# Kernel optimization log

Hardware: AMD Instinct MI355X
Metric: run time of the kernel (lower is better)

The kernel has to match this reference:

```python
import jax, jax.numpy as jnp
import numpy as np

B, S, H, NH = 2, 2048, 2048, 16
HD = H // NH  # 128


def setup_inputs() -> dict:
    key = jax.random.key(0)
    ks = jax.random.split(key, 6)
    x = jax.random.normal(ks[0], (B, S, H), dtype=jnp.float32)
    # causal additive mask: 0 on/below diagonal, -1e9 above
    causal = jnp.triu(jnp.full((S, S), -1e9, dtype=jnp.float32), k=1)
    attention_mask = causal[None, None, :, :]  # [1,1,S,S]
    # ALiBi: per-head slope * key position, broadcast over queries
    slopes = 2.0 ** (-8.0 * (jnp.arange(NH, dtype=jnp.float32) + 1) / NH)
    alibi = (-slopes[:, None] * jnp.arange(S, dtype=jnp.float32)[None, :])
    alibi = alibi[None, :, None, :]  # [1,NH,1,S]
    scale = 0.02
    Wq = jax.random.normal(ks[1], (H, H), dtype=jnp.float32) * scale
    Wk = jax.random.normal(ks[2], (H, H), dtype=jnp.float32) * scale
    Wv = jax.random.normal(ks[3], (H, H), dtype=jnp.float32) * scale
    Wo = jax.random.normal(ks[4], (H, H), dtype=jnp.float32) * scale
    return {"x": x, "attention_mask": attention_mask, "alibi": alibi,
            "Wq": Wq, "Wk": Wk, "Wv": Wv, "Wo": Wo}


def reference(x, attention_mask, alibi, Wq, Wk, Wv, Wo):
    b, s, _ = x.shape
    # nn.Linear(y) = y @ W.T
    q = (x @ Wq.T).reshape(b, s, NH, HD).transpose(0, 2, 1, 3)  # [b,h,s,d]
    k = (x @ Wk.T).reshape(b, s, NH, HD).transpose(0, 2, 1, 3)
    v = (x @ Wv.T).reshape(b, s, NH, HD).transpose(0, 2, 1, 3)
    scores = jnp.einsum('bhqd,bhkd->bhqk', q, k) / jnp.sqrt(jnp.float32(HD))
    scores = scores + alibi + attention_mask
    attn = jax.nn.softmax(scores, axis=-1)
    out = jnp.einsum('bhqk,bhkd->bhqd', attn, v)
    out = out.transpose(0, 2, 1, 3).reshape(b, s, H)
    return out @ Wo.T
```

## Files before the change

### kernel.cpp

```cpp
#include <hip/hip_runtime.h>

typedef unsigned short u16;
typedef float f32x4 __attribute__((ext_vector_type(4)));
typedef short s16x8 __attribute__((ext_vector_type(8)));
typedef short s16x4 __attribute__((ext_vector_type(4)));
typedef unsigned short u16x4 __attribute__((ext_vector_type(4)));

#define S_LEN 2048
#define HDIM 2048
#define NHEADS 16
#define HEAD_DIM 128

__device__ __forceinline__ u16 f2bf(float f) {
    unsigned u = __builtin_bit_cast(unsigned, f);
    u += 0x7FFFu + ((u >> 16) & 1u);
    return (u16)(u >> 16);
}

__device__ __forceinline__ void gload_lds16(const u16* g, u16* l) {
    __builtin_amdgcn_global_load_lds(
        (const __attribute__((address_space(1))) unsigned int*)(const void*)g,
        (__attribute__((address_space(3))) unsigned int*)(void*)l, 16, 0, 0);
}

#define PBAR __builtin_amdgcn_s_barrier()
#define SGB0 __builtin_amdgcn_sched_barrier(0)

__device__ __forceinline__ void tr_read16(const u16* bptr, s16x4* o) {
    auto p = (const __attribute__((address_space(3))) u16*)(const void*)bptr;
    asm volatile(
        "ds_read_b64_tr_b16 %0, %16\n\t"
        "ds_read_b64_tr_b16 %1, %16 offset:1024\n\t"
        "ds_read_b64_tr_b16 %2, %16 offset:128\n\t"
        "ds_read_b64_tr_b16 %3, %16 offset:1152\n\t"
        "ds_read_b64_tr_b16 %4, %16 offset:256\n\t"
        "ds_read_b64_tr_b16 %5, %16 offset:1280\n\t"
        "ds_read_b64_tr_b16 %6, %16 offset:384\n\t"
        "ds_read_b64_tr_b16 %7, %16 offset:1408\n\t"
        "ds_read_b64_tr_b16 %8, %16 offset:512\n\t"
        "ds_read_b64_tr_b16 %9, %16 offset:1536\n\t"
        "ds_read_b64_tr_b16 %10, %16 offset:640\n\t"
        "ds_read_b64_tr_b16 %11, %16 offset:1664\n\t"
        "ds_read_b64_tr_b16 %12, %16 offset:768\n\t"
        "ds_read_b64_tr_b16 %13, %16 offset:1792\n\t"
        "ds_read_b64_tr_b16 %14, %16 offset:896\n\t"
        "ds_read_b64_tr_b16 %15, %16 offset:1920\n\t"
        "s_waitcnt lgkmcnt(0)"
        : "=&v"(o[0]), "=&v"(o[1]), "=&v"(o[2]), "=&v"(o[3]),
          "=&v"(o[4]), "=&v"(o[5]), "=&v"(o[6]), "=&v"(o[7]),
          "=&v"(o[8]), "=&v"(o[9]), "=&v"(o[10]), "=&v"(o[11]),
          "=&v"(o[12]), "=&v"(o[13]), "=&v"(o[14]), "=&v"(o[15])
        : "v"(p));
    __builtin_amdgcn_sched_barrier(0);
}

__global__ void cvt_bf16(const float* __restrict__ in, u16* __restrict__ out, int n4, float scale) {
    int i = blockIdx.x * blockDim.x + threadIdx.x;
    int stride = gridDim.x * blockDim.x;
    for (; i < n4; i += stride) {
        float4 f = ((const float4*)in)[i];
        u16x4 r;
        r.x = f2bf(f.x * scale); r.y = f2bf(f.y * scale);
        r.z = f2bf(f.z * scale); r.w = f2bf(f.w * scale);
        *(u16x4*)(out + (size_t)i * 4) = r;
    }
}

__global__ void cvt_w4(const float* __restrict__ w0, const float* __restrict__ w1,
                       const float* __restrict__ w2, const float* __restrict__ w3,
                       u16* __restrict__ out, float scale0) {
    const int n4each = (HDIM * HDIM) / 4;
    int b = blockIdx.x;
    int which = b >> 11;
    const float* src = which == 0 ? w0 : which == 1 ? w1 : which == 2 ? w2 : w3;
    float sc = which == 0 ? scale0 : 1.0f;
    u16* dst = out + (size_t)which * (HDIM * HDIM);
    int i = (b & 2047) * 256 + threadIdx.x;
    const int stride = 2048 * 256;
    for (; i < n4each; i += stride) {
        float4 f = ((const float4*)src)[i];
        u16x4 r;
        r.x = f2bf(f.x * sc); r.y = f2bf(f.y * sc);
        r.z = f2bf(f.z * sc); r.w = f2bf(f.w * sc);
        *(u16x4*)(dst + (size_t)i * 4) = r;
    }
}

template<int OUT_F32>
__global__ __launch_bounds__(512, 2) void gemm_ring(const u16* __restrict__ A, const u16* __restrict__ Bw,
                                                    void* __restrict__ C0, void* __restrict__ C1,
                                                    void* __restrict__ C2, int M, int N, int K) {
    __shared__ u16 lds[3 * 24576];

    const int bid = blockIdx.x;
    const int xcd = bid & 7;
    const int q = bid >> 3;
    const int rr = q & 31, sc0 = q >> 5;
    const int bm = xcd * 4 + (rr & 3);
    const int bn = sc0 * 8 + (rr >> 2);

    const int t = threadIdx.x, lane = t & 63, w = t >> 6;
    const int wm = w >> 2, wn = w & 3;
    const int rqg = lane >> 4, rl = lane & 15;

    const size_t rowA0 = (size_t)bm * 128;
    const int colB0 = bn << 8;

    const u16* srcA[2]; int dA[2];
#pragma unroll
    for (int i = 0; i < 2; ++i) {
        int c = t + i * 512;
        int row = c >> 3, ch = c & 7;
        srcA[i] = A + (rowA0 + row) * (size_t)K + ((ch ^ (row & 7)) << 3);
        dA[i] = c * 8;
    }
    const u16* srcB[4]; int dB[4];
#pragma unroll
    for (int i = 0; i < 4; ++i) {
        int c = t + i * 512;
        int row = c >> 3, ch = c & 7;
        srcB[i] = Bw + (size_t)(colB0 + row) * (size_t)K + ((ch ^ (row & 7)) << 3);
        dB[i] = c * 8;
    }

    auto stage = [&](int tile, int s) {
        const size_t go = (size_t)tile * 64;
        u16* base = &lds[s * 24576];
#pragma unroll
        for (int i = 0; i < 2; ++i) gload_lds16(srcA[i] + go, base + dA[i]);
#pragma unroll
        for (int i = 0; i < 4; ++i) gload_lds16(srcB[i] + go, base + 8192 + dB[i]);
    };

    const int chv[2] = { ((0 + rqg) ^ (rl & 7)) << 3, ((4 + rqg) ^ (rl & 7)) << 3 };
    const int arow = wm * 64, brow = wn * 64;

    f32x4 acc[4][4] = {};

    const int NT = K >> 6;

    stage(0, 0); stage(1, 1);
    asm volatile("s_waitcnt vmcnt(6)" ::: "memory");
    PBAR;

    int s = 0;
    for (int tt = 0; tt < NT; ++tt) {
        const u16* sA = &lds[s * 24576];
        const u16* sB = sA + 8192;

        s16x8 af[4][2], bf[4][2];
#pragma unroll
        for (int m = 0; m < 4; ++m)
#pragma unroll
            for (int k = 0; k < 2; ++k)
                af[m][k] = *(const s16x8*)&sA[(arow + m * 16 + rl) * 64 + chv[k]];
#pragma unroll
        for (int n = 0; n < 4; ++n)
#pragma unroll
            for (int k = 0; k < 2; ++k)
                bf[n][k] = *(const s16x8*)&sB[(brow + n * 16 + rl) * 64 + chv[k]];

        int s2 = s + 2; if (s2 >= 3) s2 -= 3;
        if (tt + 2 < NT) stage(tt + 2, s2);
        SGB0;

        __builtin_amdgcn_s_setprio(1);
#pragma unroll
        for (int m = 0; m < 4; ++m)
#pragma unroll
            for (int n = 0; n < 4; ++n)
#pragma unroll
                for (int k = 0; k < 2; ++k)
                    acc[m][n] = __builtin_amdgcn_mfma_f32_16x16x32_bf16(af[m][k], bf[n][k], acc[m][n], 0, 0, 0);
        __builtin_amdgcn_s_setprio(0);

        if (tt + 2 < NT)      { asm volatile("s_waitcnt vmcnt(6)" ::: "memory"); }
        else if (tt + 1 < NT) { asm volatile("s_waitcnt vmcnt(0)" ::: "memory"); }
        PBAR;
        ++s; if (s == 3) s = 0;
    }

    const int mat = colB0 >> 11;
    void* Csel = mat == 0 ? C0 : mat == 1 ? C1 : C2;
    const int colb = (colB0 & 2047) + wn * 64;
#pragma unroll
    for (int m = 0; m < 4; ++m) {
#pragma unroll
        for (int n = 0; n < 4; ++n) {
#pragma unroll
            for (int j = 0; j < 4; ++j) {
                size_t row = rowA0 + wm * 64 + m * 16 + rqg * 4 + j;
                size_t col = colb + n * 16 + rl;
                float v = acc[m][n][j];
                if (OUT_F32) ((float*)Csel)[row * 2048 + col] = v;
                else ((u16*)Csel)[row * 2048 + col] = f2bf(v);
            }
        }
    }
}

__global__ __launch_bounds__(512) void attn_kernel(const u16* __restrict__ Q, const u16* __restrict__ Kb,
                                                   const u16* __restrict__ Vb,
                                                   const float* __restrict__ alibi,
                                                   u16* __restrict__ O) {
    __shared__ u16 ldsKV[3 * 16384];
    __shared__ u16 lP[8][16 * 80];

    const int bid = blockIdx.x;
    const int bh = bid & 31;
    const int p = bid >> 5;
    const int h = bh & 15, b = bh >> 4;
    const int t = threadIdx.x, lane = t & 63, w = t >> 6;
    const int rqg = lane >> 4, rl = lane & 15;

    const size_t bS = (size_t)b * S_LEN;
    const size_t hOff = (size_t)h * HEAD_DIM;

    const u16* ksrc[2]; const u16* vsrc[2]; int cdst[2];
#pragma unroll
    for (int i = 0; i < 2; ++i) {
        int c = t + i * 512;
        int krow = c >> 4, kch = c & 15;
        ksrc[i] = Kb + (bS + krow) * HDIM + hOff + ((kch ^ (krow & 7)) << 3);
        int vkey = ((c >> 6) << 2) + ((c >> 1) & 3);
        int vd = (((c >> 3) & 7) << 4) + ((c & 1) << 3);
        vsrc[i] = Vb + (bS + vkey) * HDIM + hOff + vd;
        cdst[i] = c * 8;
    }

    auto stageKV = [&](int tile, int s) {
        const size_t goff = (size_t)tile * 64 * HDIM;
        u16* base = &ldsKV[s * 16384];
#pragma unroll
        for (int i = 0; i < 2; ++i) {
            gload_lds16(ksrc[i] + goff, base + cdst[i]);
            gload_lds16(vsrc[i] + goff, base + 8192 + cdst[i]);
        }
    };

    const float mslope2 = alibi[(size_t)h * S_LEN + 1] * 1.4426950408889634f;

    s16x8 ones;
#pragma unroll
    for (int i = 0; i < 8; ++i) ones[i] = (short)0x3F80;

    for (int sidx = 0; sidx < 2; ++sidx) {
        const int qt = sidx ? (15 - p) : p;
        const int q0w = qt * 128 + w * 16;

        const size_t baseQ = (bS + q0w + rl) * HDIM + hOff;
        s16x8 qf[4];
#pragma unroll
        for (int kk = 0; kk < 4; ++kk)
            qf[kk] = *(const s16x8*)(Q + baseQ + kk * 32 + rqg * 8);

        float m[4];
        f32x4 o[8]; f32x4 osum = {0.f, 0.f, 0.f, 0.f};
#pragma unroll
        for (int j = 0; j < 4; ++j) m[j] = -1e30f;
#pragma unroll
        for (int n = 0; n < 8; ++n) o[n] = (f32x4){0.f, 0.f, 0.f, 0.f};

        const int nkt = 2 * qt + 2;
        const int my_last = 2 * qt + (w >> 2);
        u16* lPw = lP[w];

        stageKV(0, 0); stageKV(1, 1);
        asm volatile("s_waitcnt vmcnt(4)" ::: "memory");
        PBAR;

        int s = 0;
        for (int kt = 0; kt < nkt; ++kt) {
            int s2 = s + 2; if (s2 >= 3) s2 -= 3;
            if (kt + 2 < nkt) stageKV(kt + 2, s2);

            if (kt <= my_last) {
                const int k0 = kt * 64;
                const u16* kbase = &ldsKV[s * 16384];

                f32x4 sfr[4] = {};
#pragma unroll
                for (int kk = 0; kk < 4; ++kk) {
#pragma unroll
                    for (int nt = 0; nt < 4; ++nt) {
                        int row = nt * 16 + rl;
                        int off = row * 256 + ((kk * 64 + rqg * 16) ^ ((row & 7) << 4));
                        s16x8 kf = *(const s16x8*)((const char*)kbase + off);
                        sfr[nt] = __builtin_amdgcn_mfma_f32_16x16x32_bf16(qf[kk], kf, sfr[nt], 0, 0, 0);
                    }
                }

                const bool diag = (kt == my_last);
                float scv[4][4];
                float thr0 = m[0] + 8.f, thr1 = m[1] + 8.f, thr2 = m[2] + 8.f, thr3 = m[3] + 8.f;
                int small = 1;
#pragma unroll
                for (int nt = 0; nt < 4; ++nt) {
                    int key = k0 + nt * 16 + rl;
                    float al = mslope2 * (float)key;
#pragma unroll
                    for (int j = 0; j < 4; ++j) {
                        float v = sfr[nt][j] + al;
                        if (diag) {
                            int qrow = q0w + rqg * 4 + j;
                            v = (key <= qrow) ? v : -1e30f;
                        }
                        scv[nt][j] = v;
                        float thr = (j == 0) ? thr0 : (j == 1) ? thr1 : (j == 2) ? thr2 : thr3;
                        small &= (v <= thr) ? 1 : 0;
                    }
                }
                if (!__all(small)) {
                    float rmax[4];
#pragma unroll
                    for (int j = 0; j < 4; ++j)
                        rmax[j] = fmaxf(fmaxf(scv[0][j], scv[1][j]), fmaxf(scv[2][j], scv[3][j]));
#pragma unroll
                    for (int off = 1; off < 16; off <<= 1) {
#pragma unroll
                        for (int j = 0; j < 4; ++j) rmax[j] = fmaxf(rmax[j], __shfl_xor(rmax[j], off));
                    }
#pragma unroll
                    for (int j = 0; j < 4; ++j) {
                        float mn = fmaxf(m[j], rmax[j]);
                        float fac = exp2f(m[j] - mn);
                        m[j] = mn;
                        osum[j] *= fac;
#pragma unroll
                        for (int n = 0; n < 8; ++n) o[n][j] *= fac;
                    }
                }

#pragma unroll
                for (int nt = 0; nt < 4; ++nt) {
#pragma unroll
                    for (int j = 0; j < 4; ++j) {
                        float pv = exp2f(scv[nt][j] - m[j]);
                        lPw[(rqg * 4 + j) * 80 + nt * 16 + rl] = f2bf(pv);
                    }
                }

                const u16* lVbase = &ldsKV[s * 16384] + 8192 + rqg * 1024 + rl * 4;
#pragma unroll
                for (int kk = 0; kk < 2; ++kk) {
                    s16x8 pf = *(const s16x8*)&lPw[rl * 80 + kk * 32 + rqg * 8];
                    osum = __builtin_amdgcn_mfma_f32_16x16x32_bf16(pf, ones, osum, 0, 0, 0);
                    s16x4 tr[16];
                    tr_read16(lVbase + kk * 4096, tr);
#pragma unroll
                    for (int n = 0; n < 8; ++n) {
                        s16x8 vf = __builtin_shufflevector(tr[2 * n], tr[2 * n + 1], 0, 1, 2, 3, 4, 5, 6, 7);
                        o[n] = __builtin_amdgcn_mfma_f32_16x16x32_bf16(pf, vf, o[n], 0, 0, 0);
                    }
                }
            }

            if (kt + 2 < nkt)      { asm volatile("s_waitcnt vmcnt(4)" ::: "memory"); }
            else if (kt + 1 < nkt) { asm volatile("s_waitcnt vmcnt(0)" ::: "memory"); }
            PBAR;
            ++s; if (s == 3) s = 0;
        }

        float inv[4];
#pragma unroll
        for (int j = 0; j < 4; ++j) inv[j] = 1.0f / osum[j];
#pragma unroll
        for (int n = 0; n < 8; ++n) {
#pragma unroll
            for (int j = 0; j < 4; ++j) {
                size_t row = bS + q0w + rqg * 4 + j;
                O[row * HDIM + hOff + n * 16 + rl] = f2bf(o[n][j] * inv[j]);
            }
        }
    }
}

extern "C" void kernel_launch(void* const* d_in, const int* in_sizes, int n_in,
                              void* d_out, int out_size, void* d_ws, size_t ws_size,
                              hipStream_t stream) {
    (void)in_sizes; (void)n_in; (void)out_size; (void)ws_size;
    const float* x     = (const float*)d_in[0];
    const float* alibi = (const float*)d_in[2];
    const float* Wq    = (const float*)d_in[3];
    const float* Wk    = (const float*)d_in[4];
    const float* Wv    = (const float*)d_in[5];
    const float* Wo    = (const float*)d_in[6];
    float* out = (float*)d_out;

    char* ws = (char*)d_ws;
    u16* xb  = (u16*)(ws + 0);
    u16* wqb = (u16*)(ws + 16777216);
    u16* Qb  = (u16*)(ws + 50331648);
    u16* Kv  = Qb + 8388608;
    u16* Vv  = Kv + 8388608;
    u16* Ob  = Vv + 8388608;
    u16* wob = wqb + 3 * 4194304;

    const int M = 2 * S_LEN;
    const int K = HDIM;

    const float qscale = 0.08838834764831845f * 1.4426950408889634f;
    cvt_bf16<<<4096, 256, 0, stream>>>(x, xb, (2 * S_LEN * HDIM) / 4, 1.0f);
    cvt_w4<<<8192, 256, 0, stream>>>(Wq, Wk, Wv, Wo, wqb, qscale);

    gemm_ring<0><<<(M / 128) * (3 * HDIM / 256), 512, 0, stream>>>(xb, wqb, Qb, Kv, Vv, M, 3 * HDIM, K);

    attn_kernel<<<2 * NHEADS * 8, 512, 0, stream>>>(Qb, Kv, Vv, alibi, Ob);

    gemm_ring<1><<<(M / 128) * (HDIM / 256), 512, 0, stream>>>(Ob, wob, out, out, out, M, HDIM, K);
}
```

Measured before the change: 254.2 us.

## Switch GEMM to 256x128 tiles with intra-block split-K across warp halves

Changes the GEMM block tile from 128x256 to 256x128 and splits the 64-wide K slice between two groups of four waves, each computing a 128x64 sub-tile over half the K chunk. The partial sums from the second group are reduced through LDS before the epilogue. The prefetch for the next stage is also issued before the fragment loads, with an explicit lgkmcnt wait. This halves the number of fragment loads per MFMA relative to accumulator size and raises accumulator registers per wave, at the cost of an LDS reduction and a barrier at the end, plus a changed block-to-XCD mapping.

```diff
diff --git a/kernel.cpp b/kernel.cpp
--- a/kernel.cpp
+++ b/kernel.cpp
@@ -95,47 +95,47 @@
     const int bid = blockIdx.x;
     const int xcd = bid & 7;
     const int q = bid >> 3;
-    const int rr = q & 31, sc0 = q >> 5;
-    const int bm = xcd * 4 + (rr & 3);
-    const int bn = sc0 * 8 + (rr >> 2);
+    const int bm = xcd * 2 + (q & 1);
+    const int bn = q >> 1;
 
     const int t = threadIdx.x, lane = t & 63, w = t >> 6;
-    const int wm = w >> 2, wn = w & 3;
+    const int kk = w >> 2;
+    const int wm = (w >> 1) & 1, wn = w & 1;
     const int rqg = lane >> 4, rl = lane & 15;
 
-    const size_t rowA0 = (size_t)bm * 128;
-    const int colB0 = bn << 8;
-
-    const u16* srcA[2]; int dA[2];
-#pragma unroll
-    for (int i = 0; i < 2; ++i) {
+    const size_t rowA0 = (size_t)bm * 256;
+    const int colB0 = bn << 7;
+
+    const u16* srcA[4]; int dA[4];
+#pragma unroll
+    for (int i = 0; i < 4; ++i) {
         int c = t + i * 512;
         int row = c >> 3, ch = c & 7;
         srcA[i] = A + (rowA0 + row) * (size_t)K + ((ch ^ (row & 7)) << 3);
         dA[i] = c * 8;
     }
-    const u16* srcB[4]; int dB[4];
-#pragma unroll
-    for (int i = 0; i < 4; ++i) {
+    const u16* srcB[2]; int dB[2];
+#pragma unroll
+    for (int i = 0; i < 2; ++i) {
         int c = t + i * 512;
         int row = c >> 3, ch = c & 7;
         srcB[i] = Bw + (size_t)(colB0 + row) * (size_t)K + ((ch ^ (row & 7)) << 3);
-        dB[i] = c * 8;
+        dB[i] = 16384 + c * 8;
     }
 
     auto stage = [&](int tile, int s) {
         const size_t go = (size_t)tile * 64;
         u16* base = &lds[s * 24576];
 #pragma unroll
-        for (int i = 0; i < 2; ++i) gload_lds16(srcA[i] + go, base + dA[i]);
-#pragma unroll
-        for (int i = 0; i < 4; ++i) gload_lds16(srcB[i] + go, base + 8192 + dB[i]);
+        for (int i = 0; i < 4; ++i) gload_lds16(srcA[i] + go, base + dA[i]);
+#pragma unroll
+        for (int i = 0; i < 2; ++i) gload_lds16(srcB[i] + go, base + dB[i]);
     };
 
-    const int chv[2] = { ((0 + rqg) ^ (rl & 7)) << 3, ((4 + rqg) ^ (rl & 7)) << 3 };
-    const int arow = wm * 64, brow = wn * 64;
-
-    f32x4 acc[4][4] = {};
+    const int chf = ((kk * 4 + rqg) ^ (rl & 7)) << 3;
+    const int arowb = wm * 128, browb = wn * 64;
+
+    f32x4 acc[8][4] = {};
 
     const int NT = K >> 6;
 
@@ -145,33 +145,29 @@
 
     int s = 0;
     for (int tt = 0; tt < NT; ++tt) {
-        const u16* sA = &lds[s * 24576];
-        const u16* sB = sA + 8192;
-
-        s16x8 af[4][2], bf[4][2];
-#pragma unroll
-        for (int m = 0; m < 4; ++m)
-#pragma unroll
-            for (int k = 0; k < 2; ++k)
-                af[m][k] = *(const s16x8*)&sA[(arow + m * 16 + rl) * 64 + chv[k]];
-#pragma unroll
-        for (int n = 0; n < 4; ++n)
-#pragma unroll
-            for (int k = 0; k < 2; ++k)
-                bf[n][k] = *(const s16x8*)&sB[(brow + n * 16 + rl) * 64 + chv[k]];
-
         int s2 = s + 2; if (s2 >= 3) s2 -= 3;
         if (tt + 2 < NT) stage(tt + 2, s2);
+
+        const u16* sA = &lds[s * 24576];
+        const u16* sB = sA + 16384;
+
+        s16x8 af[8], bf[4];
+#pragma unroll
+        for (int m = 0; m < 8; ++m)
+            af[m] = *(const s16x8*)&sA[(arowb + m * 16 + rl) * 64 + chf];
+#pragma unroll
+        for (int n = 0; n < 4; ++n)
+            bf[n] = *(const s16x8*)&sB[(browb + n * 16 + rl) * 64 + chf];
+
+        asm volatile("s_waitcnt lgkmcnt(0)" ::: "memory");
         SGB0;
 
         __builtin_amdgcn_s_setprio(1);
 #pragma unroll
-        for (int m = 0; m < 4; ++m)
+        for (int m = 0; m < 8; ++m)
 #pragma unroll
             for (int n = 0; n < 4; ++n)
-#pragma unroll
-                for (int k = 0; k < 2; ++k)
-                    acc[m][n] = __builtin_amdgcn_mfma_f32_16x16x32_bf16(af[m][k], bf[n][k], acc[m][n], 0, 0, 0);
+                acc[m][n] = __builtin_amdgcn_mfma_f32_16x16x32_bf16(af[m], bf[n], acc[m][n], 0, 0, 0);
         __builtin_amdgcn_s_setprio(0);
 
         if (tt + 2 < NT)      { asm volatile("s_waitcnt vmcnt(6)" ::: "memory"); }
@@ -180,20 +176,31 @@
         ++s; if (s == 3) s = 0;
     }
 
-    const int mat = colB0 >> 11;
-    void* Csel = mat == 0 ? C0 : mat == 1 ? C1 : C2;
-    const int colb = (colB0 & 2047) + wn * 64;
-#pragma unroll
-    for (int m = 0; m < 4; ++m) {
-#pragma unroll
-        for (int n = 0; n < 4; ++n) {
-#pragma unroll
-            for (int j = 0; j < 4; ++j) {
-                size_t row = rowA0 + wm * 64 + m * 16 + rqg * 4 + j;
-                size_t col = colb + n * 16 + rl;
-                float v = acc[m][n][j];
-                if (OUT_F32) ((float*)Csel)[row * 2048 + col] = v;
-                else ((u16*)Csel)[row * 2048 + col] = f2bf(v);
+    float* fb = (float*)lds;
+    if (kk == 1) {
+#pragma unroll
+        for (int m = 0; m < 8; ++m)
+#pragma unroll
+            for (int n = 0; n < 4; ++n)
+                *(f32x4*)&fb[(w & 3) * 8192 + (m * 4 + n) * 256 + lane * 4] = acc[m][n];
+    }
+    __syncthreads();
+    if (kk == 0) {
+        const int mat = colB0 >> 11;
+        void* Csel = mat == 0 ? C0 : mat == 1 ? C1 : C2;
+        const int colb = (colB0 & 2047) + wn * 64;
+#pragma unroll
+        for (int m = 0; m < 8; ++m) {
+#pragma unroll
+            for (int n = 0; n < 4; ++n) {
+                f32x4 v = acc[m][n] + *(const f32x4*)&fb[w * 8192 + (m * 4 + n) * 256 + lane * 4];
+#pragma unroll
+                for (int j = 0; j < 4; ++j) {
+                    size_t row = rowA0 + wm * 128 + m * 16 + rqg * 4 + j;
+                    size_t col = colb + n * 16 + rl;
+                    if (OUT_F32) ((float*)Csel)[row * 2048 + col] = v[j];
+                    else ((u16*)Csel)[row * 2048 + col] = f2bf(v[j]);
+                }
             }
         }
     }
@@ -403,9 +410,9 @@
     cvt_bf16<<<4096, 256, 0, stream>>>(x, xb, (2 * S_LEN * HDIM) / 4, 1.0f);
     cvt_w4<<<8192, 256, 0, stream>>>(Wq, Wk, Wv, Wo, wqb, qscale);
 
-    gemm_ring<0><<<(M / 128) * (3 * HDIM / 256), 512, 0, stream>>>(xb, wqb, Qb, Kv, Vv, M, 3 * HDIM, K);
+    gemm_ring<0><<<(M / 256) * (3 * HDIM / 128), 512, 0, stream>>>(xb, wqb, Qb, Kv, Vv, M, 3 * HDIM, K);
 
     attn_kernel<<<2 * NHEADS * 8, 512, 0, stream>>>(Qb, Kv, Vv, alibi, Ob);
 
-    gemm_ring<1><<<(M / 128) * (HDIM / 256), 512, 0, stream>>>(Ob, wob, out, out, out, M, HDIM, K);
-}
+    gemm_ring<1><<<(M / 256) * (HDIM / 128), 512, 0, stream>>>(Ob, wob, out, out, out, M, HDIM, K);
+}
```

After: 257.8 us. Within noise of the previous version (+1.4%).

## Add dedicated QKV GEMM with 256x192 tiles and double-buffered LDS

Applied to the files above, without the earlier changes.

Splits the templated GEMM into a QKV-specific kernel and an output-projection kernel. The QKV kernel uses 256x192 block tiles with a 4x2 wave layout (64x96 per wave), double-buffered LDS, and an XCD-aware block mapping. The grid becomes 16x32=512 blocks, which may fill the 256 CUs more evenly and gives more reuse per loaded byte. It also adds explicit lgkmcnt waits plus a barrier before refilling the buffer, which could serialize LDS reads and global loads more than the old three-stage ring did.

```diff
diff --git a/kernel.cpp b/kernel.cpp
--- a/kernel.cpp
+++ b/kernel.cpp
@@ -86,10 +86,118 @@
     }
 }
 
-template<int OUT_F32>
-__global__ __launch_bounds__(512, 2) void gemm_ring(const u16* __restrict__ A, const u16* __restrict__ Bw,
-                                                    void* __restrict__ C0, void* __restrict__ C1,
-                                                    void* __restrict__ C2, int M, int N, int K) {
+__global__ __launch_bounds__(512, 2) void gemm_qkv(const u16* __restrict__ A, const u16* __restrict__ Bw,
+                                                   u16* __restrict__ C0, u16* __restrict__ C1,
+                                                   u16* __restrict__ C2, int M, int N, int K) {
+    __shared__ u16 lds[2][28672];
+
+    const int bid = blockIdx.x;
+    const int xcd = bid & 7;
+    const int q = bid >> 3;
+    const int bm = xcd * 2 + (q & 1);
+    const int bn = q >> 1;
+
+    const int t = threadIdx.x, lane = t & 63, w = t >> 6;
+    const int wm = w >> 1, wn = w & 1;
+    const int rqg = lane >> 4, rl = lane & 15;
+
+    const size_t rowA0 = (size_t)bm * 256;
+    const int colB0 = bn * 192;
+
+    const u16* srcA[4]; int dA[4];
+#pragma unroll
+    for (int i = 0; i < 4; ++i) {
+        int c = t + i * 512;
+        int row = c >> 3, ch = c & 7;
+        srcA[i] = A + (rowA0 + row) * (size_t)K + ((ch ^ (row & 7)) << 3);
+        dA[i] = c * 8;
+    }
+    const u16* srcB[3]; int dB[3];
+#pragma unroll
+    for (int i = 0; i < 3; ++i) {
+        int c = t + i * 512;
+        int row = c >> 3, ch = c & 7;
+        srcB[i] = Bw + (size_t)(colB0 + row) * (size_t)K + ((ch ^ (row & 7)) << 3);
+        dB[i] = 16384 + c * 8;
+    }
+
+    auto stage = [&](int tile, int side) {
+        const size_t go = (size_t)tile * 64;
+        u16* base = &lds[side][0];
+#pragma unroll
+        for (int i = 0; i < 4; ++i) gload_lds16(srcA[i] + go, base + dA[i]);
+#pragma unroll
+        for (int i = 0; i < 3; ++i) gload_lds16(srcB[i] + go, base + dB[i]);
+    };
+
+    const int chv[2] = { ((0 + rqg) ^ (rl & 7)) << 3, ((4 + rqg) ^ (rl & 7)) << 3 };
+    const int arow = wm * 64, brow = wn * 96;
+
+    f32x4 acc[4][6] = {};
+
+    const int NT = K >> 6;
+
+    stage(0, 0); stage(1, 1);
+    asm volatile("s_waitcnt vmcnt(7)" ::: "memory");
+    PBAR;
+
+    for (int tt = 0; tt < NT; ++tt) {
+        const int side = tt & 1;
+        const u16* sA = &lds[side][0];
+        const u16* sB = sA + 16384;
+
+        s16x8 af[4][2], bf[6][2];
+#pragma unroll
+        for (int m = 0; m < 4; ++m)
+#pragma unroll
+            for (int k = 0; k < 2; ++k)
+                af[m][k] = *(const s16x8*)&sA[(arow + m * 16 + rl) * 64 + chv[k]];
+#pragma unroll
+        for (int n = 0; n < 6; ++n)
+#pragma unroll
+            for (int k = 0; k < 2; ++k)
+                bf[n][k] = *(const s16x8*)&sB[(brow + n * 16 + rl) * 64 + chv[k]];
+
+        asm volatile("s_waitcnt lgkmcnt(0)" ::: "memory");
+        SGB0;
+        PBAR;
+        SGB0;
+        if (tt + 2 < NT) stage(tt + 2, side);
+
+        __builtin_amdgcn_s_setprio(1);
+#pragma unroll
+        for (int m = 0; m < 4; ++m)
+#pragma unroll
+            for (int n = 0; n < 6; ++n)
+#pragma unroll
+                for (int k = 0; k < 2; ++k)
+                    acc[m][n] = __builtin_amdgcn_mfma_f32_16x16x32_bf16(af[m][k], bf[n][k], acc[m][n], 0, 0, 0);
+        __builtin_amdgcn_s_setprio(0);
+
+        if (tt + 2 < NT)      { asm volatile("s_waitcnt vmcnt(7)" ::: "memory"); }
+        else if (tt + 1 < NT) { asm volatile("s_waitcnt vmcnt(0)" ::: "memory"); }
+        PBAR;
+    }
+
+#pragma unroll
+    for (int m = 0; m < 4; ++m) {
+#pragma unroll
+        for (int n = 0; n < 6; ++n) {
+            int colg = colB0 + wn * 96 + n * 16;
+            int mat = colg >> 11;
+            u16* Csel = mat == 0 ? C0 : mat == 1 ? C1 : C2;
+            int colm = (colg & 2047) + rl;
+#pragma unroll
+            for (int j = 0; j < 4; ++j) {
+                size_t row = rowA0 + wm * 64 + m * 16 + rqg * 4 + j;
+                Csel[row * 2048 + colm] = f2bf(acc[m][n][j]);
+            }
+        }
+    }
+}
+
+__global__ __launch_bounds__(512, 2) void gemm_wo(const u16* __restrict__ A, const u16* __restrict__ Bw,
+                                                  float* __restrict__ C, int M, int N, int K) {
     __shared__ u16 lds[3 * 24576];
 
     const int bid = blockIdx.x;
@@ -163,6 +271,8 @@
         int s2 = s + 2; if (s2 >= 3) s2 -= 3;
         if (tt + 2 < NT) stage(tt + 2, s2);
         SGB0;
+        asm volatile("s_waitcnt lgkmcnt(0)" ::: "memory");
+        SGB0;
 
         __builtin_amdgcn_s_setprio(1);
 #pragma unroll
@@ -180,9 +290,6 @@
         ++s; if (s == 3) s = 0;
     }
 
-    const int mat = colB0 >> 11;
-    void* Csel = mat == 0 ? C0 : mat == 1 ? C1 : C2;
-    const int colb = (colB0 & 2047) + wn * 64;
 #pragma unroll
     for (int m = 0; m < 4; ++m) {
 #pragma unroll
@@ -190,10 +297,8 @@
 #pragma unroll
             for (int j = 0; j < 4; ++j) {
                 size_t row = rowA0 + wm * 64 + m * 16 + rqg * 4 + j;
-                size_t col = colb + n * 16 + rl;
-                float v = acc[m][n][j];
-                if (OUT_F32) ((float*)Csel)[row * 2048 + col] = v;
-                else ((u16*)Csel)[row * 2048 + col] = f2bf(v);
+                size_t col = colB0 + wn * 64 + n * 16 + rl;
+                C[row * 2048 + col] = acc[m][n][j];
             }
         }
     }
@@ -403,9 +508,9 @@
     cvt_bf16<<<4096, 256, 0, stream>>>(x, xb, (2 * S_LEN * HDIM) / 4, 1.0f);
     cvt_w4<<<8192, 256, 0, stream>>>(Wq, Wk, Wv, Wo, wqb, qscale);
 
-    gemm_ring<0><<<(M / 128) * (3 * HDIM / 256), 512, 0, stream>>>(xb, wqb, Qb, Kv, Vv, M, 3 * HDIM, K);
+    gemm_qkv<<<(M / 256) * (3 * HDIM / 192), 512, 0, stream>>>(xb, wqb, Qb, Kv, Vv, M, 3 * HDIM, K);
 
     attn_kernel<<<2 * NHEADS * 8, 512, 0, stream>>>(Qb, Kv, Vv, alibi, Ob);
 
-    gemm_ring<1><<<(M / 128) * (HDIM / 256), 512, 0, stream>>>(Ob, wob, out, out, out, M, HDIM, K);
-}
+    gemm_wo<<<(M / 128) * (HDIM / 256), 512, 0, stream>>>(Ob, wob, out, M, HDIM, K);
+}
```

Result: faster. 243.4 us (-4.2%).

## Shrink attention blocks to 64-query tiles with double-buffered KV staging

Applied to the files above, without the earlier changes.

The attention kernel moves from 512-thread blocks covering 128 query rows to 256-thread blocks covering 64 rows, and doubles the grid to 512 blocks with two blocks per CU allowed. The three-stage KV ring is replaced by a two-buffer scheme with a full vmcnt(0) wait each iteration. Each warp now stops exactly at its diagonal tile, so the per-warp skip logic for the last KV tile is gone. This aims to improve load balance and occupancy, and it halves LDS use per block. In exchange, prefetch depth is shallower, and each KV tile is loaded from global memory by twice as many blocks.

```diff
diff --git a/kernel.cpp b/kernel.cpp
--- a/kernel.cpp
+++ b/kernel.cpp
@@ -199,12 +199,12 @@
     }
 }
 
-__global__ __launch_bounds__(512) void attn_kernel(const u16* __restrict__ Q, const u16* __restrict__ Kb,
-                                                   const u16* __restrict__ Vb,
-                                                   const float* __restrict__ alibi,
-                                                   u16* __restrict__ O) {
-    __shared__ u16 ldsKV[3 * 16384];
-    __shared__ u16 lP[8][16 * 80];
+__global__ __launch_bounds__(256, 2) void attn_kernel(const u16* __restrict__ Q, const u16* __restrict__ Kb,
+                                                      const u16* __restrict__ Vb,
+                                                      const float* __restrict__ alibi,
+                                                      u16* __restrict__ O) {
+    __shared__ u16 ldsKV[2][16384];
+    __shared__ u16 lP[4][16 * 80];
 
     const int bid = blockIdx.x;
     const int bh = bid & 31;
@@ -216,10 +216,10 @@
     const size_t bS = (size_t)b * S_LEN;
     const size_t hOff = (size_t)h * HEAD_DIM;
 
-    const u16* ksrc[2]; const u16* vsrc[2]; int cdst[2];
-#pragma unroll
-    for (int i = 0; i < 2; ++i) {
-        int c = t + i * 512;
+    const u16* ksrc[4]; const u16* vsrc[4]; int cdst[4];
+#pragma unroll
+    for (int i = 0; i < 4; ++i) {
+        int c = t + i * 256;
         int krow = c >> 4, kch = c & 15;
         ksrc[i] = Kb + (bS + krow) * HDIM + hOff + ((kch ^ (krow & 7)) << 3);
         int vkey = ((c >> 6) << 2) + ((c >> 1) & 3);
@@ -228,11 +228,11 @@
         cdst[i] = c * 8;
     }
 
-    auto stageKV = [&](int tile, int s) {
+    auto stageKV = [&](int tile, int side) {
         const size_t goff = (size_t)tile * 64 * HDIM;
-        u16* base = &ldsKV[s * 16384];
-#pragma unroll
-        for (int i = 0; i < 2; ++i) {
+        u16* base = &ldsKV[side][0];
+#pragma unroll
+        for (int i = 0; i < 4; ++i) {
             gload_lds16(ksrc[i] + goff, base + cdst[i]);
             gload_lds16(vsrc[i] + goff, base + 8192 + cdst[i]);
         }
@@ -245,8 +245,8 @@
     for (int i = 0; i < 8; ++i) ones[i] = (short)0x3F80;
 
     for (int sidx = 0; sidx < 2; ++sidx) {
-        const int qt = sidx ? (15 - p) : p;
-        const int q0w = qt * 128 + w * 16;
+        const int qt = sidx ? (31 - p) : p;
+        const int q0w = qt * 64 + w * 16;
 
         const size_t baseQ = (bS + q0w + rl) * HDIM + hOff;
         s16x8 qf[4];
@@ -261,104 +261,98 @@
 #pragma unroll
         for (int n = 0; n < 8; ++n) o[n] = (f32x4){0.f, 0.f, 0.f, 0.f};
 
-        const int nkt = 2 * qt + 2;
-        const int my_last = 2 * qt + (w >> 2);
+        const int nkt = qt + 1;
         u16* lPw = lP[w];
 
-        stageKV(0, 0); stageKV(1, 1);
-        asm volatile("s_waitcnt vmcnt(4)" ::: "memory");
+        stageKV(0, 0);
+        asm volatile("s_waitcnt vmcnt(0)" ::: "memory");
         PBAR;
 
-        int s = 0;
         for (int kt = 0; kt < nkt; ++kt) {
-            int s2 = s + 2; if (s2 >= 3) s2 -= 3;
-            if (kt + 2 < nkt) stageKV(kt + 2, s2);
-
-            if (kt <= my_last) {
-                const int k0 = kt * 64;
-                const u16* kbase = &ldsKV[s * 16384];
-
-                f32x4 sfr[4] = {};
-#pragma unroll
-                for (int kk = 0; kk < 4; ++kk) {
-#pragma unroll
-                    for (int nt = 0; nt < 4; ++nt) {
-                        int row = nt * 16 + rl;
-                        int off = row * 256 + ((kk * 64 + rqg * 16) ^ ((row & 7) << 4));
-                        s16x8 kf = *(const s16x8*)((const char*)kbase + off);
-                        sfr[nt] = __builtin_amdgcn_mfma_f32_16x16x32_bf16(qf[kk], kf, sfr[nt], 0, 0, 0);
+            const int side = kt & 1;
+            if (kt + 1 < nkt) stageKV(kt + 1, side ^ 1);
+
+            const int k0 = kt * 64;
+            const u16* kbase = &ldsKV[side][0];
+
+            f32x4 sfr[4] = {};
+#pragma unroll
+            for (int kk = 0; kk < 4; ++kk) {
+#pragma unroll
+                for (int nt = 0; nt < 4; ++nt) {
+                    int row = nt * 16 + rl;
+                    int off = row * 256 + ((kk * 64 + rqg * 16) ^ ((row & 7) << 4));
+                    s16x8 kf = *(const s16x8*)((const char*)kbase + off);
+                    sfr[nt] = __builtin_amdgcn_mfma_f32_16x16x32_bf16(qf[kk], kf, sfr[nt], 0, 0, 0);
+                }
+            }
+
+            const bool diag = (kt == qt);
+            float scv[4][4];
+            float thr0 = m[0] + 8.f, thr1 = m[1] + 8.f, thr2 = m[2] + 8.f, thr3 = m[3] + 8.f;
+            int small = 1;
+#pragma unroll
+            for (int nt = 0; nt < 4; ++nt) {
+                int key = k0 + nt * 16 + rl;
+                float al = mslope2 * (float)key;
+#pragma unroll
+                for (int j = 0; j < 4; ++j) {
+                    float v = sfr[nt][j] + al;
+                    if (diag) {
+                        int qrow = q0w + rqg * 4 + j;
+                        v = (key <= qrow) ? v : -1e30f;
                     }
-                }
-
-                const bool diag = (kt == my_last);
-                float scv[4][4];
-                float thr0 = m[0] + 8.f, thr1 = m[1] + 8.f, thr2 = m[2] + 8.f, thr3 = m[3] + 8.f;
-                int small = 1;
-#pragma unroll
-                for (int nt = 0; nt < 4; ++nt) {
-                    int key = k0 + nt * 16 + rl;
-                    float al = mslope2 * (float)key;
-#pragma unroll
-                    for (int j = 0; j < 4; ++j) {
-                        float v = sfr[nt][j] + al;
-                        if (diag) {
-                            int qrow = q0w + rqg * 4 + j;
-                            v = (key <= qrow) ? v : -1e30f;
-                        }
-                        scv[nt][j] = v;
-                        float thr = (j == 0) ? thr0 : (j == 1) ? thr1 : (j == 2) ? thr2 : thr3;
-                        small &= (v <= thr) ? 1 : 0;
-                    }
-                }
-                if (!__all(small)) {
-                    float rmax[4];
-#pragma unroll
-                    for (int j = 0; j < 4; ++j)
-                        rmax[j] = fmaxf(fmaxf(scv[0][j], scv[1][j]), fmaxf(scv[2][j], scv[3][j]));
-#pragma unroll
-                    for (int off = 1; off < 16; off <<= 1) {
-#pragma unroll
-                        for (int j = 0; j < 4; ++j) rmax[j] = fmaxf(rmax[j], __shfl_xor(rmax[j], off));
-                    }
-#pragma unroll
-                    for (int j = 0; j < 4; ++j) {
-                        float mn = fmaxf(m[j], rmax[j]);
-                        float fac = exp2f(m[j] - mn);
-                        m[j] = mn;
-                        osum[j] *= fac;
-#pragma unroll
-                        for (int n = 0; n < 8; ++n) o[n][j] *= fac;
-                    }
-                }
-
-#pragma unroll
-                for (int nt = 0; nt < 4; ++nt) {
-#pragma unroll
-                    for (int j = 0; j < 4; ++j) {
-                        float pv = exp2f(scv[nt][j] - m[j]);
-                        lPw[(rqg * 4 + j) * 80 + nt * 16 + rl] = f2bf(pv);
-                    }
-                }
-
-                const u16* lVbase = &ldsKV[s * 16384] + 8192 + rqg * 1024 + rl * 4;
-#pragma unroll
-                for (int kk = 0; kk < 2; ++kk) {
-                    s16x8 pf = *(const s16x8*)&lPw[rl * 80 + kk * 32 + rqg * 8];
-                    osum = __builtin_amdgcn_mfma_f32_16x16x32_bf16(pf, ones, osum, 0, 0, 0);
-                    s16x4 tr[16];
-                    tr_read16(lVbase + kk * 4096, tr);
-#pragma unroll
-                    for (int n = 0; n < 8; ++n) {
-                        s16x8 vf = __builtin_shufflevector(tr[2 * n], tr[2 * n + 1], 0, 1, 2, 3, 4, 5, 6, 7);
-                        o[n] = __builtin_amdgcn_mfma_f32_16x16x32_bf16(pf, vf, o[n], 0, 0, 0);
-                    }
-                }
-            }
-
-            if (kt + 2 < nkt)      { asm volatile("s_waitcnt vmcnt(4)" ::: "memory"); }
-            else if (kt + 1 < nkt) { asm volatile("s_waitcnt vmcnt(0)" ::: "memory"); }
+                    scv[nt][j] = v;
+                    float thr = (j == 0) ? thr0 : (j == 1) ? thr1 : (j == 2) ? thr2 : thr3;
+                    small &= (v <= thr) ? 1 : 0;
+                }
+            }
+            if (!__all(small)) {
+                float rmax[4];
+#pragma unroll
+                for (int j = 0; j < 4; ++j)
+                    rmax[j] = fmaxf(fmaxf(scv[0][j], scv[1][j]), fmaxf(scv[2][j], scv[3][j]));
+#pragma unroll
+                for (int off = 1; off < 16; off <<= 1) {
+#pragma unroll
+                    for (int j = 0; j < 4; ++j) rmax[j] = fmaxf(rmax[j], __shfl_xor(rmax[j], off));
+                }
+#pragma unroll
+                for (int j = 0; j < 4; ++j) {
+                    float mn = fmaxf(m[j], rmax[j]);
+                    float fac = exp2f(m[j] - mn);
+                    m[j] = mn;
+                    osum[j] *= fac;
+#pragma unroll
+                    for (int n = 0; n < 8; ++n) o[n][j] *= fac;
+                }
+            }
+
+#pragma unroll
+            for (int nt = 0; nt < 4; ++nt) {
+#pragma unroll
+                for (int j = 0; j < 4; ++j) {
+                    float pv = exp2f(scv[nt][j] - m[j]);
+                    lPw[(rqg * 4 + j) * 80 + nt * 16 + rl] = f2bf(pv);
+                }
+            }
+
+            const u16* lVbase = &ldsKV[side][0] + 8192 + rqg * 1024 + rl * 4;
+#pragma unroll
+            for (int kk = 0; kk < 2; ++kk) {
+                s16x8 pf = *(const s16x8*)&lPw[rl * 80 + kk * 32 + rqg * 8];
+                osum = __builtin_amdgcn_mfma_f32_16x16x32_bf16(pf, ones, osum, 0, 0, 0);
+                s16x4 tr[16];
+                tr_read16(lVbase + kk * 4096, tr);
+#pragma unroll
+                for (int n = 0; n < 8; ++n) {
+                    s16x8 vf = __builtin_shufflevector(tr[2 * n], tr[2 * n + 1], 0, 1, 2, 3, 4, 5, 6, 7);
+                    o[n] = __builtin_amdgcn_mfma_f32_16x16x32_bf16(pf, vf, o[n], 0, 0, 0);
+                }
+            }
+
+            asm volatile("s_waitcnt vmcnt(0)" ::: "memory");
             PBAR;
-            ++s; if (s == 3) s = 0;
         }
 
         float inv[4];
@@ -405,7 +399,7 @@
 
     gemm_ring<0><<<(M / 128) * (3 * HDIM / 256), 512, 0, stream>>>(xb, wqb, Qb, Kv, Vv, M, 3 * HDIM, K);
 
-    attn_kernel<<<2 * NHEADS * 8, 512, 0, stream>>>(Qb, Kv, Vv, alibi, Ob);
+    attn_kernel<<<2 * NHEADS * 16, 256, 0, stream>>>(Qb, Kv, Vv, alibi, Ob);
 
     gemm_ring<1><<<(M / 128) * (HDIM / 256), 512, 0, stream>>>(Ob, wob, out, out, out, M, HDIM, K);
 }
```

New measurement: 251.2 us. Within noise of the previous version (-1.2%).
